# Kernel optimization log

Measured on AMD Instinct MI355X. Metric: run time of the kernel, lower is better.

The kernel has to match this reference:

```python
import jax, jax.numpy as jnp
import numpy as np

NUM_HEADS = 8
RMS_EPS = 1e-8


def rmsnorm(x, g):
    return x * jax.lax.rsqrt(jnp.mean(x * x, axis=-1, keepdims=True) + RMS_EPS) * g


def activation_quant(x):
    # per-token int8 absmax quant
    scale = 127.0 / jnp.clip(jnp.max(jnp.abs(x), axis=-1, keepdims=True), 1e-5)
    return jnp.clip(jnp.round(x * scale), -128, 127) / scale


def weight_quant(w):
    # ternary (1.58-bit) mean-absmax quant
    scale = 1.0 / jnp.clip(jnp.mean(jnp.abs(w)), 1e-5)
    return jnp.clip(jnp.round(w * scale), -1, 1) / scale


def bitlinear(x, w, g):
    # BitLinear: RMSNorm -> STE-quantized activation @ STE-quantized ternary weight
    xn = rmsnorm(x, g)
    xq = xn + jax.lax.stop_gradient(activation_quant(xn) - xn)
    wq = w + jax.lax.stop_gradient(weight_quant(w) - w)
    return xq @ wq.T


def _attention_pass(q_in, ctx, Wq, gq, Wkv, gkv, A, Bm, mag, Wp, gp):
    B, Nq, C = q_in.shape
    H = NUM_HEADS
    hd = C // H
    scale = hd ** -0.5
    q_proj = bitlinear(q_in, Wq, gq)                       # [B,Nq,C]
    delta = (q_in @ A.T) @ Bm.T                            # DoRA low-rank delta [B,Nq,C]
    q = q_proj.reshape(B, Nq, H, hd).transpose(0, 2, 1, 3)  # [B,H,Nq,hd]
    d = delta.reshape(B, Nq, H, hd).transpose(0, 2, 1, 3)
    q_final = q + mag * d                                  # mag: [1,H,1,1]
    kv = bitlinear(ctx, Wkv, gkv)                          # [B,Nc,2C]
    k, v = jnp.split(kv, 2, axis=-1)
    Nc = ctx.shape[1]
    k = k.reshape(B, Nc, H, hd).transpose(0, 2, 1, 3)
    v = v.reshape(B, Nc, H, hd).transpose(0, 2, 1, 3)
    scores = jnp.einsum('bhqd,bhkd->bhqk', q_final, k) * scale
    out = jnp.einsum('bhqk,bhkd->bhqd', jax.nn.softmax(scores, axis=-1), v)
    out = out.transpose(0, 2, 1, 3).reshape(B, Nq, C)
    return bitlinear(out, Wp, gp)


def setup_inputs() -> dict:
    key = jax.random.key(0)
    ks = jax.random.split(key, 20)
    B, Nx, Nc, D, R = 4, 4096, 1024, 512, 16
    H = NUM_HEADS

    def rn(k, shape, s=0.02):
        return jax.random.normal(k, shape, dtype=jnp.float32) * s

    return {
        'x': jax.random.normal(ks[0], (B, Nx, D), dtype=jnp.float32),
        'c': jax.random.normal(ks[1], (B, Nc, D), dtype=jnp.float32),
        # x-queries-on-c pass
        'W_qx': rn(ks[2], (D, D)), 'g_qx': jnp.ones((D,), jnp.float32),
        'W_kvc': rn(ks[3], (2 * D, D)), 'g_kvc': jnp.ones((D,), jnp.float32),
        'A_x': rn(ks[4], (R, D)), 'B_x': rn(ks[5], (D, R)),
        'mag_x': jnp.ones((1, H, 1, 1), jnp.float32),
        'W_px': rn(ks[6], (D, D)), 'g_px': jnp.ones((D,), jnp.float32),
        # c-queries-on-x pass
        'W_qc': rn(ks[7], (D, D)), 'g_qc': jnp.ones((D,), jnp.float32),
        'W_kvx': rn(ks[8], (2 * D, D)), 'g_kvx': jnp.ones((D,), jnp.float32),
        'A_c': rn(ks[9], (R, D)), 'B_c': rn(ks[10], (D, R)),
        'mag_c': jnp.ones((1, H, 1, 1), jnp.float32),
        'W_pc': rn(ks[11], (D, D)), 'g_pc': jnp.ones((D,), jnp.float32),
    }


def reference(x, c, W_qx, g_qx, W_kvc, g_kvc, A_x, B_x, mag_x, W_px, g_px,
              W_qc, g_qc, W_kvx, g_kvx, A_c, B_c, mag_c, W_pc, g_pc):
    x_out = x + _attention_pass(x, c, W_qx, g_qx, W_kvc, g_kvc, A_x, B_x, mag_x, W_px, g_px)
    c_out = c + _attention_pass(c, x, W_qc, g_qc, W_kvx, g_kvx, A_c, B_c, mag_c, W_pc, g_pc)
    return (x_out, c_out)
```

## Files before the change

### kernel.cpp

```cpp
#include <hip/hip_runtime.h>
#include <math.h>

#define DD 512
#define NHEAD 8
#define HDIM 64

typedef __bf16 bf16x8 __attribute__((ext_vector_type(8)));
typedef unsigned short u16x8 __attribute__((ext_vector_type(8)));
typedef float f32x4 __attribute__((ext_vector_type(4)));

#if __has_builtin(__builtin_amdgcn_exp2f)
#define EXP2F(x) __builtin_amdgcn_exp2f(x)
#else
#define EXP2F(x) exp2f(x)
#endif

#define QSCALE 0.18033688f

static __device__ __forceinline__ unsigned short f2bf(float f) {
    unsigned u = __builtin_bit_cast(unsigned, f);
    u += 0x7fffu + ((u >> 16) & 1u);
    return (unsigned short)(u >> 16);
}
static __device__ __forceinline__ float bf2f(unsigned short u) {
    return __builtin_bit_cast(float, (unsigned)u << 16);
}

static __device__ __forceinline__ float wsum32(const float* __restrict__ part, int mid) {
    int l = threadIdx.x & 63;
    float v = (l < 32) ? part[mid * 32 + l] : 0.f;
#pragma unroll
    for (int o = 16; o > 0; o >>= 1) v += __shfl_xor(v, o);
    return __shfl(v, 0);
}

#define GLOAD16(g, l)                                                          \
    __builtin_amdgcn_global_load_lds(                                          \
        (__attribute__((address_space(1))) void*)(g),                          \
        (__attribute__((address_space(3))) void*)(l), 16, 0, 0)

#define BSTEP(s, hc)                                                           \
    {                                                                          \
        _Pragma("unroll")                                                      \
        for (int i = 0; i < (hc); ++i) {                                       \
            float send = (lane & (s)) ? p[i] : p[i + (hc)];                    \
            float recv = __shfl_xor(send, (s));                                \
            p[i] = ((lane & (s)) ? p[i + (hc)] : p[i]) + recv;                 \
        }                                                                      \
    }

#define GEMM_KLOOP(Aq, Wq, m0, n0)                                             \
    {                                                                          \
        _Pragma("unroll")                                                      \
        for (int i = 0; i < 2; ++i) {                                          \
            int row = i * 64 + row_st;                                         \
            GLOAD16(Aq + (size_t)((m0) + row) * 512 + chunk * 8,               \
                    sA[0] + ((size_t)i * 256 + t) * 8);                        \
            GLOAD16(Wq + (size_t)((n0) + row) * 512 + chunk * 8,               \
                    sB[0] + ((size_t)i * 256 + t) * 8);                        \
        }                                                                      \
        asm volatile("s_waitcnt vmcnt(0)" ::: "memory");                       \
        __syncthreads();                                                       \
        int cur = 0;                                                           \
        for (int k0 = 0; k0 < 512; k0 += 32) {                                 \
            if (k0 + 32 < 512) {                                               \
                _Pragma("unroll")                                              \
                for (int i = 0; i < 2; ++i) {                                  \
                    int row = i * 64 + row_st;                                 \
                    GLOAD16(Aq + (size_t)((m0) + row) * 512 + k0 + 32 + chunk * 8, \
                            sA[cur ^ 1] + ((size_t)i * 256 + t) * 8);          \
                    GLOAD16(Wq + (size_t)((n0) + row) * 512 + k0 + 32 + chunk * 8, \
                            sB[cur ^ 1] + ((size_t)i * 256 + t) * 8);          \
                }                                                              \
            }                                                                  \
            bf16x8 af[4], bfr[4];                                              \
            _Pragma("unroll")                                                  \
            for (int mt = 0; mt < 4; ++mt)                                     \
                af[mt] = *reinterpret_cast<const bf16x8*>(                     \
                    &sA[cur][(wm * 64 + mt * 16 + lr) * 32 + lg * 8]);         \
            _Pragma("unroll")                                                  \
            for (int nt = 0; nt < 4; ++nt)                                     \
                bfr[nt] = *reinterpret_cast<const bf16x8*>(                    \
                    &sB[cur][(wn * 64 + nt * 16 + lr) * 32 + lg * 8]);         \
            __builtin_amdgcn_s_setprio(1);                                     \
            _Pragma("unroll")                                                  \
            for (int mt = 0; mt < 4; ++mt)                                     \
                _Pragma("unroll")                                              \
                for (int nt = 0; nt < 4; ++nt)                                 \
                    acc[mt][nt] = __builtin_amdgcn_mfma_f32_16x16x32_bf16(     \
                        af[mt], bfr[nt], acc[mt][nt], 0, 0, 0);                \
            __builtin_amdgcn_s_setprio(0);                                     \
            asm volatile("s_waitcnt vmcnt(0)" ::: "memory");                   \
            __syncthreads();                                                   \
            cur ^= 1;                                                          \
        }                                                                      \
    }

__global__ __launch_bounds__(256) void k_prep1(
    const float* __restrict__ W0, const float* __restrict__ W1,
    const float* __restrict__ W2, const float* __restrict__ W3,
    const float* __restrict__ W4, const float* __restrict__ W5,
    float* __restrict__ part,
    const float* __restrict__ x, const float* __restrict__ c,
    const float* __restrict__ g_qx, const float* __restrict__ g_kvx,
    const float* __restrict__ g_qc, const float* __restrict__ g_kvc,
    unsigned short* __restrict__ a_xq, unsigned short* __restrict__ a_xkv,
    unsigned short* __restrict__ a_cq, unsigned short* __restrict__ a_ckv,
    float* __restrict__ s_xq, float* __restrict__ s_xkv,
    float* __restrict__ s_cq, float* __restrict__ s_ckv,
    const float* __restrict__ A_x, const float* __restrict__ A_c,
    float* __restrict__ tmp_x, float* __restrict__ tmp_c) {
    int t = threadIdx.x;
    if (blockIdx.x < 192) {
        const float* Ws[6] = {W0, W1, W2, W3, W4, W5};
        const int cnt[6] = {262144, 524288, 262144, 262144, 524288, 262144};
        int mid = blockIdx.x >> 5, lb = blockIdx.x & 31;
        const float* W = Ws[mid];
        int n = cnt[mid];
        float s = 0.f;
        for (int i = lb * 256 + t; i < n; i += 32 * 256) s += fabsf(W[i]);
        __shared__ float red[4];
#pragma unroll
        for (int o = 32; o > 0; o >>= 1) s += __shfl_down(s, o);
        if ((t & 63) == 0) red[t >> 6] = s;
        __syncthreads();
        if (t == 0) part[blockIdx.x] = red[0] + red[1] + red[2] + red[3];
        return;
    }
    int w = t >> 6, lane = t & 63;
    int row = (int)(blockIdx.x - 192) * 4 + w;
    bool pc = (row >= 16384);
    int r = pc ? row - 16384 : row;
    const float* xr = (pc ? c : x) + (size_t)r * DD;
    const float* G1 = pc ? g_qc : g_qx;
    const float* G2 = pc ? g_kvc : g_kvx;
    unsigned short* O1 = pc ? a_cq : a_xq;
    unsigned short* O2 = pc ? a_ckv : a_xkv;
    float* S1 = pc ? s_cq : s_xq;
    float* S2 = pc ? s_ckv : s_xkv;
    const float* AM = pc ? A_c : A_x;
    float* TMP = pc ? tmp_c : tmp_x;

    float4 a = *(const float4*)(xr + lane * 8);
    float4 b = *(const float4*)(xr + lane * 8 + 4);
    float p[16];
#pragma unroll
    for (int cc = 0; cc < 16; ++cc) {
        const float4* ar = (const float4*)(AM + (size_t)cc * DD + lane * 8);
        float4 aa = ar[0], ab = ar[1];
        p[cc] = a.x*aa.x + a.y*aa.y + a.z*aa.z + a.w*aa.w
              + b.x*ab.x + b.y*ab.y + b.z*ab.z + b.w*ab.w;
    }
    BSTEP(1, 8) BSTEP(2, 4) BSTEP(4, 2) BSTEP(8, 1)
    p[0] += __shfl_xor(p[0], 16);
    p[0] += __shfl_xor(p[0], 32);
    if (lane < 16) {
        int cidx = ((lane & 1) << 3) | ((lane & 2) << 1) | ((lane & 4) >> 1) | ((lane & 8) >> 3);
        TMP[(size_t)r * 16 + cidx] = p[0];
    }
    float ss = a.x*a.x + a.y*a.y + a.z*a.z + a.w*a.w
             + b.x*b.x + b.y*b.y + b.z*b.z + b.w*b.w;
#pragma unroll
    for (int o = 32; o > 0; o >>= 1) ss += __shfl_xor(ss, o);
    float rn = 1.f / sqrtf(ss * (1.f / 512.f) + 1e-8f);
    const float* gs[2] = {G1, G2};
    unsigned short* os[2] = {O1, O2};
    float* scs[2] = {S1, S2};
#pragma unroll
    for (int pass = 0; pass < 2; ++pass) {
        float4 ga = *(const float4*)(gs[pass] + lane * 8);
        float4 gb = *(const float4*)(gs[pass] + lane * 8 + 4);
        float v[8] = {a.x*rn*ga.x, a.y*rn*ga.y, a.z*rn*ga.z, a.w*rn*ga.w,
                      b.x*rn*gb.x, b.y*rn*gb.y, b.z*rn*gb.z, b.w*rn*gb.w};
        float amax = 0.f;
#pragma unroll
        for (int i = 0; i < 8; ++i) amax = fmaxf(amax, fabsf(v[i]));
#pragma unroll
        for (int o = 32; o > 0; o >>= 1) amax = fmaxf(amax, __shfl_xor(amax, o));
        float mx = fmaxf(amax, 1e-5f);
        float scale = 127.f / mx;
        u16x8 qv;
#pragma unroll
        for (int i = 0; i < 8; ++i) {
            float tq = rintf(v[i] * scale);
            tq = fminf(fmaxf(tq, -128.f), 127.f);
            qv[i] = f2bf(tq);
        }
        *reinterpret_cast<u16x8*>(os[pass] + (size_t)r * DD + lane * 8) = qv;
        if (lane == 0) scs[pass][r] = mx / 127.f;
    }
}

__global__ __launch_bounds__(256) void k_prep2(
    const float* __restrict__ W0, const float* __restrict__ W1,
    const float* __restrict__ W2, const float* __restrict__ W3,
    const float* __restrict__ W4, const float* __restrict__ W5,
    const float* __restrict__ part, unsigned short* __restrict__ Wq,
    const float* __restrict__ tmp_x, const float* __restrict__ tmp_c,
    const float* __restrict__ B_x, const float* __restrict__ B_c,
    unsigned short* __restrict__ qf1, unsigned short* __restrict__ qf2) {
    if (blockIdx.x < 8192) {
        int e = blockIdx.x * 256 + threadIdx.x;
        const float* Ws[6] = {W0, W1, W2, W3, W4, W5};
        int mid, base;
        if (e < 262144)       { mid = 0; base = 0; }
        else if (e < 786432)  { mid = 1; base = 262144; }
        else if (e < 1048576) { mid = 2; base = 786432; }
        else if (e < 1310720) { mid = 3; base = 1048576; }
        else if (e < 1835008) { mid = 4; base = 1310720; }
        else                  { mid = 5; base = 1835008; }
        float cnt = (mid == 1 || mid == 4) ? 524288.f : 262144.f;
        float mean = fmaxf(wsum32(part, mid) / cnt, 1e-5f);
        float sc = 1.f / mean;
        float t = rintf(Ws[mid][e - base] * sc);
        t = fminf(fmaxf(t, -1.f), 1.f);
        Wq[e] = f2bf(t);
        return;
    }
    int idx = (int)(blockIdx.x - 8192) * 256 + threadIdx.x;
    int m2 = idx >> 9, n2 = idx & 511;
    const float* tr;
    const float* br;
    unsigned short* out;
    if (m2 < 16384) {
        tr = tmp_x + (size_t)m2 * 16; br = B_x + (size_t)n2 * 16; out = qf1 + idx;
    } else {
        tr = tmp_c + (size_t)(m2 - 16384) * 16; br = B_c + (size_t)n2 * 16;
        out = qf2 + (idx - 8388608);
    }
    const float4* t4 = (const float4*)tr;
    const float4* b4 = (const float4*)br;
    float acc = 0.f;
#pragma unroll
    for (int rr = 0; rr < 4; ++rr) {
        float4 ta = t4[rr], ba = b4[rr];
        acc += ta.x*ba.x + ta.y*ba.y + ta.z*ba.z + ta.w*ba.w;
    }
    *out = f2bf(acc);
}

__global__ __launch_bounds__(256) void k_rmsq_combine(
    const unsigned short* __restrict__ Op_a, const float* __restrict__ Lp_a,
    const float* __restrict__ g_a, unsigned short* __restrict__ out_a,
    float* __restrict__ sc_a,
    const unsigned short* __restrict__ Op_b, const float* __restrict__ Lp_b,
    const float* __restrict__ g_b, unsigned short* __restrict__ out_b,
    float* __restrict__ sc_b) {
    int w = threadIdx.x >> 6, lane = threadIdx.x & 63;
    int row = (int)blockIdx.x * 4 + w;
    bool pb = (row >= 16384);
    int r = pb ? row - 16384 : row;
    int S = pb ? 4 : 1;
    int lognq = pb ? 10 : 12;
    const unsigned short* Op = pb ? Op_b : Op_a;
    const float* Lp = pb ? Lp_b : Lp_a;
    const float* g  = pb ? g_b : g_a;
    unsigned short* out = pb ? out_b : out_a;
    float* a_inv = pb ? sc_b : sc_a;

    int Nq = 1 << lognq;
    int b = r >> lognq, q = r & (Nq - 1);
    int h = lane >> 3;
    float l = 0.f;
    float u[8] = {};
    for (int s = 0; s < S; ++s) {
        l += Lp[((size_t)(s * 4 + b) * 8 + h) * Nq + q];
        u16x8 ov = *reinterpret_cast<const u16x8*>(
            Op + ((size_t)(s * 4 + b) * Nq + q) * 512 + lane * 8);
#pragma unroll
        for (int i = 0; i < 8; ++i) u[i] += bf2f(ov[i]);
    }
    float invl = 1.f / l;
#pragma unroll
    for (int i = 0; i < 8; ++i) u[i] *= invl;
    float ss = 0.f;
#pragma unroll
    for (int i = 0; i < 8; ++i) ss += u[i] * u[i];
#pragma unroll
    for (int o = 32; o > 0; o >>= 1) ss += __shfl_xor(ss, o);
    float rn = 1.f / sqrtf(ss * (1.f / 512.f) + 1e-8f);
    float4 ga = *(const float4*)(g + lane * 8);
    float4 gb = *(const float4*)(g + lane * 8 + 4);
    float v[8] = {u[0]*rn*ga.x, u[1]*rn*ga.y, u[2]*rn*ga.z, u[3]*rn*ga.w,
                  u[4]*rn*gb.x, u[5]*rn*gb.y, u[6]*rn*gb.z, u[7]*rn*gb.w};
    float amax = 0.f;
#pragma unroll
    for (int i = 0; i < 8; ++i) amax = fmaxf(amax, fabsf(v[i]));
#pragma unroll
    for (int o = 32; o > 0; o >>= 1) amax = fmaxf(amax, __shfl_xor(amax, o));
    float mx = fmaxf(amax, 1e-5f);
    float scale = 127.f / mx;
    u16x8 qv;
#pragma unroll
    for (int i = 0; i < 8; ++i) {
        float tq = rintf(v[i] * scale);
        tq = fminf(fmaxf(tq, -128.f), 127.f);
        qv[i] = f2bf(tq);
    }
    *reinterpret_cast<u16x8*>(out + (size_t)r * DD + lane * 8) = qv;
    if (lane == 0) a_inv[r] = mx / 127.f;
}

__global__ __launch_bounds__(256) void k_gemm_qkv(
    const unsigned short* __restrict__ a3_a, const unsigned short* __restrict__ a3_b,
    const unsigned short* __restrict__ w3_a, const unsigned short* __restrict__ w3_b,
    const float* __restrict__ ai3_a, const float* __restrict__ ai3_b,
    const float* __restrict__ mag_a, const float* __restrict__ mag_b,
    const unsigned short* __restrict__ dl_a, const unsigned short* __restrict__ dl_b,
    unsigned short* __restrict__ Qb_a, unsigned short* __restrict__ Qb_b,
    const unsigned short* __restrict__ a4_a, const unsigned short* __restrict__ a4_b,
    const unsigned short* __restrict__ w4_a, const unsigned short* __restrict__ w4_b,
    const float* __restrict__ ai4_a, const float* __restrict__ ai4_b,
    unsigned short* __restrict__ Kb_a, unsigned short* __restrict__ Kb_b,
    unsigned short* __restrict__ Vt_a, unsigned short* __restrict__ Vt_b,
    const float* __restrict__ part) {
    __shared__ __align__(16) unsigned short sA[2][128 * 32];
    __shared__ __align__(16) unsigned short sB[2][128 * 32];
    int bid = blockIdx.x;
    bool isQ = (bid >= 1280);
    const unsigned short *Aq, *Wq;
    const float* a_inv;
    int m0, n0, logn, mid;
    float cnt;
    bool pb;
    if (!isQ) {
        int g = bid & 7, k = bid >> 3;
        n0 = (k & 7) * 128;
        int my = (k >> 3) * 8 + g;
        pb = my >= 32;
        m0 = (pb ? my - 32 : my) * 128;
        Aq = pb ? a4_b : a4_a;  Wq = pb ? w4_b : w4_a;
        a_inv = pb ? ai4_b : ai4_a;
        logn = pb ? 12 : 10;
        mid = pb ? 4 : 1; cnt = 524288.f;
    } else {
        int b2 = bid - 1280;
        int g = b2 & 7, k = b2 >> 3;
        n0 = (k & 3) * 128;
        int my = (k >> 2) * 8 + g;
        pb = my >= 128;
        m0 = (pb ? my - 128 : my) * 128;
        Aq = pb ? a3_b : a3_a;  Wq = pb ? w3_b : w3_a;
        a_inv = pb ? ai3_b : ai3_a;
        logn = pb ? 10 : 12;
        mid = pb ? 3 : 0; cnt = 262144.f;
    }
    float wv = fmaxf(wsum32(part, mid) / cnt, 1e-5f);

    int t = threadIdx.x;
    int w = t >> 6, lane = t & 63;
    int wm = w >> 1, wn = w & 1;
    int lr = lane & 15, lg = lane >> 4;
    int row_st = t >> 2, chunk = t & 3;
    f32x4 acc[4][4] = {};

    GEMM_KLOOP(Aq, Wq, m0, n0)

    if (!isQ) {
        unsigned short* OutB = pb ? Kb_b : Kb_a;
        unsigned short* OutB2 = pb ? Vt_b : Vt_a;
        const bool isV = (n0 >= 512);
        const int Nc = 1 << logn;
#pragma unroll
        for (int mt = 0; mt < 4; ++mt) {
            int mb = m0 + wm * 64 + mt * 16 + lg * 4;
            int b = mb >> logn, key = mb & (Nc - 1);
            float as_[4];
#pragma unroll
            for (int r = 0; r < 4; ++r) as_[r] = a_inv[mb + r] * wv;
#pragma unroll
            for (int nt = 0; nt < 4; ++nt) {
                int n = n0 + wn * 64 + nt * 16 + lr;
                int n2 = isV ? (n - 512) : n;
                int h = n2 >> 6, dd = n2 & 63;
                if (isV) {
                    int i0 = key & 31;
                    int keyp = (key & ~31) | (((i0 >> 2) & 3) * 8 + ((i0 >> 4) & 1) * 4);
                    ushort4 v;
                    v.x = f2bf(acc[mt][nt][0] * as_[0]);
                    v.y = f2bf(acc[mt][nt][1] * as_[1]);
                    v.z = f2bf(acc[mt][nt][2] * as_[2]);
                    v.w = f2bf(acc[mt][nt][3] * as_[3]);
                    *reinterpret_cast<ushort4*>(
                        OutB2 + ((size_t)(b * NHEAD + h) * 64 + dd) * Nc + keyp) = v;
                } else {
#pragma unroll
                    for (int r = 0; r < 4; ++r)
                        OutB[((size_t)(b * NHEAD + h) * Nc + key + r) * 64 + dd] =
                            f2bf(acc[mt][nt][r] * as_[r]);
                }
            }
        }
    } else {
        const float* Extra = pb ? mag_b : mag_a;
        const unsigned short* Dlt = pb ? dl_b : dl_a;
        unsigned short* OutB = pb ? Qb_b : Qb_a;
#pragma unroll
        for (int mt = 0; mt < 4; ++mt) {
#pragma unroll
            for (int r = 0; r < 4; ++r) {
                int m = m0 + wm * 64 + mt * 16 + lg * 4 + r;
                float as = a_inv[m] * wv;
                int b = m >> logn, q = m & ((1 << logn) - 1);
#pragma unroll
                for (int nt = 0; nt < 4; ++nt) {
                    int n = n0 + wn * 64 + nt * 16 + lr;
                    float dl = bf2f(Dlt[(size_t)m * 512 + n]);
                    float val = acc[mt][nt][r] * as + Extra[n >> 6] * dl;
                    int h = n >> 6, d = n & 63;
                    OutB[((((size_t)(b * NHEAD + h)) << logn) + q) * 64 + d] =
                        f2bf(val * QSCALE);
                }
            }
        }
    }
}

__global__ __launch_bounds__(256) void k_gemm_out(
    const unsigned short* __restrict__ a_a, const unsigned short* __restrict__ a_b,
    const unsigned short* __restrict__ w_a, const unsigned short* __restrict__ w_b,
    const float* __restrict__ ai_a, const float* __restrict__ ai_b,
    const float* __restrict__ part,
    const float* __restrict__ Ex_a, const float* __restrict__ Ex_b,
    float* __restrict__ OF_a, float* __restrict__ OF_b) {
    __shared__ __align__(16) unsigned short sA[2][128 * 32];
    __shared__ __align__(16) unsigned short sB[2][128 * 32];
    int bid = blockIdx.x;
    int g = bid & 7, k = bid >> 3;
    int n0 = (k & 3) * 128;
    int my = (k >> 2) * 8 + g;
    bool pb = (my >= 128);
    int m0 = (pb ? my - 128 : my) * 128;
    const unsigned short* Aq = pb ? a_b : a_a;
    const unsigned short* Wq = pb ? w_b : w_a;
    const float* a_inv = pb ? ai_b : ai_a;
    const float* Extra = pb ? Ex_b : Ex_a;
    float* OutF = pb ? OF_b : OF_a;
    float wv = fmaxf(wsum32(part, pb ? 5 : 2) / 262144.f, 1e-5f);

    int t = threadIdx.x;
    int w = t >> 6, lane = t & 63;
    int wm = w >> 1, wn = w & 1;
    int lr = lane & 15, lg = lane >> 4;
    int row_st = t >> 2, chunk = t & 3;
    f32x4 acc[4][4] = {};

    GEMM_KLOOP(Aq, Wq, m0, n0)

#pragma unroll
    for (int mt = 0; mt < 4; ++mt) {
#pragma unroll
        for (int r = 0; r < 4; ++r) {
            int m = m0 + wm * 64 + mt * 16 + lg * 4 + r;
            float as = a_inv[m] * wv;
#pragma unroll
            for (int nt = 0; nt < 4; ++nt) {
                int n = n0 + wn * 64 + nt * 16 + lr;
                size_t idx = (size_t)m * 512 + n;
                OutF[idx] = acc[mt][nt][r] * as + Extra[idx];
            }
        }
    }
}

__global__ __launch_bounds__(512) void k_attn_mfma(
    const unsigned short* __restrict__ Qb_a, const unsigned short* __restrict__ Kb_a,
    const unsigned short* __restrict__ Vt_a, unsigned short* __restrict__ Op_a,
    float* __restrict__ Lp_a,
    const unsigned short* __restrict__ Qb_b, const unsigned short* __restrict__ Kb_b,
    const unsigned short* __restrict__ Vt_b, unsigned short* __restrict__ Op_b,
    float* __restrict__ Lp_b) {
    __shared__ unsigned short sK[2][64][72];
    __shared__ unsigned short sVt[2][64][72];
    int t = threadIdx.x;
    int w = t >> 6, lane = t & 63;
    int lr = lane & 15, lg = lane >> 4;

    int bid = blockIdx.x;
    bool pb = (bid < 512);
    int lb = pb ? bid : bid - 512;
    const unsigned short* Qb = pb ? Qb_b : Qb_a;
    const unsigned short* Kb = pb ? Kb_b : Kb_a;
    const unsigned short* Vt = pb ? Vt_b : Vt_a;
    unsigned short* Opart = pb ? Op_b : Op_a;
    float* Lpart = pb ? Lp_b : Lp_a;
    int Nq = pb ? 1024 : 4096;
    int Nc = pb ? 4096 : 1024;
    int S = pb ? 4 : 1;
    int LOGS = pb ? 2 : 0;
    int nqs = pb ? 2 : 4;

    int j = lb >> 3;
    int s = j & (S - 1);
    int j2 = j >> LOGS;
    int qblk = j2 & ((1 << nqs) - 1);
    int bh = ((lb & 7) << 2) | (j2 >> nqs);
    int b = bh >> 3, h = bh & 7;
    int q0 = qblk * 256 + w * 32;

    bf16x8 aq[2][2];
#pragma unroll
    for (int qt = 0; qt < 2; ++qt) {
        const unsigned short* qbase = Qb + ((size_t)bh * Nq + q0 + qt * 16 + lr) * 64 + lg * 8;
        aq[qt][0] = *reinterpret_cast<const bf16x8*>(qbase);
        aq[qt][1] = *reinterpret_cast<const bf16x8*>(qbase + 32);
    }

    u16x8 ou;
#pragma unroll
    for (int jj = 0; jj < 8; ++jj) ou[jj] = (lr == 0) ? 0x3F80 : 0;
    bf16x8 onesf = __builtin_bit_cast(bf16x8, ou);

    f32x4 o[2][4] = {};
    f32x4 osum[2] = {};

    const unsigned short* kglob = Kb + (size_t)bh * Nc * 64;
    const unsigned short* vglob = Vt + (size_t)bh * 64 * (size_t)Nc;

    int srow = t >> 3, sseg = t & 7;
    const unsigned short* kptr = kglob + (size_t)srow * 64 + sseg * 8;
    const unsigned short* vptr = vglob + (size_t)srow * Nc + sseg * 8;

    int kts = s * (Nc >> LOGS);
    int nt = (Nc >> LOGS) >> 6;

    bf16x8 rK = *reinterpret_cast<const bf16x8*>(kptr + (size_t)kts * 64);
    bf16x8 rV = *reinterpret_cast<const bf16x8*>(vptr + kts);
    *reinterpret_cast<bf16x8*>(&sK[0][srow][sseg * 8]) = rK;
    *reinterpret_cast<bf16x8*>(&sVt[0][srow][sseg * 8]) = rV;
    rK = *reinterpret_cast<const bf16x8*>(kptr + (size_t)(kts + 64) * 64);
    rV = *reinterpret_cast<const bf16x8*>(vptr + kts + 64);
    __syncthreads();

    int cur = 0;
    for (int ti = 0; ti < nt; ++ti) {
        if (ti + 1 < nt) {
            *reinterpret_cast<bf16x8*>(&sK[cur ^ 1][srow][sseg * 8]) = rK;
            *reinterpret_cast<bf16x8*>(&sVt[cur ^ 1][srow][sseg * 8]) = rV;
            if (ti + 2 < nt) {
                int knext = kts + (ti + 2) * 64;
                rK = *reinterpret_cast<const bf16x8*>(kptr + (size_t)knext * 64);
                rV = *reinterpret_cast<const bf16x8*>(vptr + knext);
            }
        }
#pragma unroll
        for (int half = 0; half < 2; ++half) {
            bf16x8 pa0, pa1;
#pragma unroll
            for (int ki = 0; ki < 2; ++ki) {
                int kt = half * 2 + ki;
                bf16x8 bk0 = *reinterpret_cast<const bf16x8*>(&sK[cur][kt * 16 + lr][lg * 8]);
                bf16x8 bk1 = *reinterpret_cast<const bf16x8*>(&sK[cur][kt * 16 + lr][32 + lg * 8]);
                f32x4 a0 = {}, a1 = {};
                __builtin_amdgcn_s_setprio(1);
                a0 = __builtin_amdgcn_mfma_f32_16x16x32_bf16(bk0, aq[0][0], a0, 0, 0, 0);
                a1 = __builtin_amdgcn_mfma_f32_16x16x32_bf16(bk0, aq[1][0], a1, 0, 0, 0);
                a0 = __builtin_amdgcn_mfma_f32_16x16x32_bf16(bk1, aq[0][1], a0, 0, 0, 0);
                a1 = __builtin_amdgcn_mfma_f32_16x16x32_bf16(bk1, aq[1][1], a1, 0, 0, 0);
                __builtin_amdgcn_s_setprio(0);
                const int hb = ki * 4;
#pragma unroll
                for (int r = 0; r < 4; ++r) {
                    pa0[hb + r] = (__bf16)EXP2F(a0[r]);
                    pa1[hb + r] = (__bf16)EXP2F(a1[r]);
                }
            }
            __builtin_amdgcn_s_setprio(1);
#pragma unroll
            for (int dt = 0; dt < 4; ++dt) {
                bf16x8 vb = *reinterpret_cast<const bf16x8*>(&sVt[cur][dt * 16 + lr][half * 32 + lg * 8]);
                o[0][dt] = __builtin_amdgcn_mfma_f32_16x16x32_bf16(pa0, vb, o[0][dt], 0, 0, 0);
                o[1][dt] = __builtin_amdgcn_mfma_f32_16x16x32_bf16(pa1, vb, o[1][dt], 0, 0, 0);
            }
            osum[0] = __builtin_amdgcn_mfma_f32_16x16x32_bf16(pa0, onesf, osum[0], 0, 0, 0);
            osum[1] = __builtin_amdgcn_mfma_f32_16x16x32_bf16(pa1, onesf, osum[1], 0, 0, 0);
            __builtin_amdgcn_s_setprio(0);
        }
        __syncthreads();
        cur ^= 1;
    }
    unsigned short* obase = Opart + ((size_t)(s * 4 + b) * Nq + q0) * 512 + h * 64;
#pragma unroll
    for (int qt = 0; qt < 2; ++qt)
#pragma unroll
        for (int dt = 0; dt < 4; ++dt)
#pragma unroll
            for (int r = 0; r < 4; ++r)
                obase[(size_t)(qt * 16 + lg * 4 + r) * 512 + dt * 16 + lr] = f2bf(o[qt][dt][r]);
    if (lr == 0) {
        float* lbase = Lpart + ((size_t)(s * 4 + b) * 8 + h) * Nq + q0;
#pragma unroll
        for (int qt = 0; qt < 2; ++qt)
#pragma unroll
            for (int r = 0; r < 4; ++r)
                lbase[qt * 16 + lg * 4 + r] = osum[qt][r];
    }
}

extern "C" void kernel_launch(void* const* d_in, const int* in_sizes, int n_in,
                              void* d_out, int out_size, void* d_ws, size_t ws_size,
                              hipStream_t stream) {
    const float* x     = (const float*)d_in[0];
    const float* c     = (const float*)d_in[1];
    const float* Wq_x  = (const float*)d_in[2];
    const float* g_qx  = (const float*)d_in[3];
    const float* Wkv_c = (const float*)d_in[4];
    const float* g_kvc = (const float*)d_in[5];
    const float* A_x   = (const float*)d_in[6];
    const float* B_x   = (const float*)d_in[7];
    const float* mag_x = (const float*)d_in[8];
    const float* Wp_x  = (const float*)d_in[9];
    const float* g_px  = (const float*)d_in[10];
    const float* Wq_c  = (const float*)d_in[11];
    const float* g_qc  = (const float*)d_in[12];
    const float* Wkv_x = (const float*)d_in[13];
    const float* g_kvx = (const float*)d_in[14];
    const float* A_c   = (const float*)d_in[15];
    const float* B_c   = (const float*)d_in[16];
    const float* mag_c = (const float*)d_in[17];
    const float* Wp_c  = (const float*)d_in[18];
    const float* g_pc  = (const float*)d_in[19];

    float* ws = (float*)d_ws;
    unsigned short* Wb = (unsigned short*)ws;
    const size_t Woff[6] = {0, 262144, 786432, 1048576, 1310720, 1835008};
    float* part  = ws + 1048576;
    float* sc_xq  = ws + 1049600;
    float* sc_xkv = sc_xq + 16384;
    float* sc_cq  = sc_xkv + 16384;
    float* sc_ckv = sc_cq + 4096;
    float* sc_o1  = sc_ckv + 4096;
    float* sc_o2  = sc_o1 + 16384;
    float* tmp_x  = ws + 1111040;
    float* tmp_c  = tmp_x + 262144;
    float* actblk = ws + 1438720;
    unsigned short* act_xq  = (unsigned short*)actblk;
    unsigned short* act_xkv = (unsigned short*)(actblk + 4194304);
    unsigned short* act_cq  = (unsigned short*)(actblk + 8388608);
    unsigned short* act_ckv = (unsigned short*)(actblk + 9437184);
    unsigned short* Opart1 = (unsigned short*)actblk;
    float* qf1_f  = ws + 11924480;
    unsigned short* Opart2 = (unsigned short*)qf1_f;
    float* qf2_f  = ws + 16118784;
    float* Qb1_f  = ws + 17167360;
    float* Qb2_f  = ws + 21361664;
    float* Kb1_f  = ws + 22410240;
    float* Vt1_f  = ws + 23458816;
    float* Kb2_f  = ws + 24507392;
    float* Vt2_f  = ws + 28701696;
    float* Lpart1 = ws + 32896000;
    float* Lpart2 = ws + 33027072;

    unsigned short* qf1 = (unsigned short*)qf1_f;
    unsigned short* qf2 = (unsigned short*)qf2_f;
    unsigned short* Qb1 = (unsigned short*)Qb1_f;
    unsigned short* Qb2 = (unsigned short*)Qb2_f;
    unsigned short* Kb1 = (unsigned short*)Kb1_f;
    unsigned short* Vt1 = (unsigned short*)Vt1_f;
    unsigned short* Kb2 = (unsigned short*)Kb2_f;
    unsigned short* Vt2 = (unsigned short*)Vt2_f;
    unsigned short* act_o1 = Qb1;
    unsigned short* act_o2 = Qb2;

    size_t need = (size_t)33158144 * sizeof(float);
    if (ws_size < need) return;

    float* outx = (float*)d_out;
    float* outc = outx + (size_t)4 * 4096 * 512;

    k_prep1<<<5312, 256, 0, stream>>>(Wq_x, Wkv_c, Wp_x, Wq_c, Wkv_x, Wp_c, part,
                                      x, c, g_qx, g_kvx, g_qc, g_kvc,
                                      act_xq, act_xkv, act_cq, act_ckv,
                                      sc_xq, sc_xkv, sc_cq, sc_ckv,
                                      A_x, A_c, tmp_x, tmp_c);
    k_prep2<<<49152, 256, 0, stream>>>(Wq_x, Wkv_c, Wp_x, Wq_c, Wkv_x, Wp_c, part, Wb,
                                       tmp_x, tmp_c, B_x, B_c, qf1, qf2);
    k_gemm_qkv<<<1920, 256, 0, stream>>>(
        act_xq, act_cq, Wb + Woff[0], Wb + Woff[3], sc_xq, sc_cq,
        mag_x, mag_c, qf1, qf2, Qb1, Qb2,
        act_ckv, act_xkv, Wb + Woff[1], Wb + Woff[4], sc_ckv, sc_xkv,
        Kb1, Kb2, Vt1, Vt2, part);
    k_attn_mfma<<<1024, 512, 0, stream>>>(Qb1, Kb1, Vt1, Opart1, Lpart1,
                                          Qb2, Kb2, Vt2, Opart2, Lpart2);
    k_rmsq_combine<<<5120, 256, 0, stream>>>(Opart1, Lpart1, g_px, act_o1, sc_o1,
                                             Opart2, Lpart2, g_pc, act_o2, sc_o2);
    k_gemm_out<<<640, 256, 0, stream>>>(
        act_o1, act_o2, Wb + Woff[2], Wb + Woff[5], sc_o1, sc_o2, part,
        x, c, outx, outc);
}
```

Baseline: 271.4 us.

## Switch BitLinear GEMMs from bf16 to int8 MFMA with int8 activations and weights

Stores quantized activations and ternary weights as int8 instead of bf16, and replaces the bf16 16x16x32 MFMA k-loop with the i32 16x16x64 int8 MFMA, using K steps of 64. This halves the global and LDS bytes per GEMM tile, halves the number of k-iterations, and uses the higher int8 matrix throughput. Integer accumulators are converted to float in the epilogues. The results stay exact because the quantized values are small integers, but the GEMMs may be only part of total time next to attention.

```diff
diff --git a/kernel.cpp b/kernel.cpp
--- a/kernel.cpp
+++ b/kernel.cpp
@@ -8,6 +8,8 @@
 typedef __bf16 bf16x8 __attribute__((ext_vector_type(8)));
 typedef unsigned short u16x8 __attribute__((ext_vector_type(8)));
 typedef float f32x4 __attribute__((ext_vector_type(4)));
+typedef int i32x4 __attribute__((ext_vector_type(4)));
+typedef signed char i8x8 __attribute__((ext_vector_type(8)));
 
 #if __has_builtin(__builtin_amdgcn_exp2f)
 #define EXP2F(x) __builtin_amdgcn_exp2f(x)
@@ -49,45 +51,43 @@
         }                                                                      \
     }
 
-#define GEMM_KLOOP(Aq, Wq, m0, n0)                                             \
+#define GEMM_KLOOP_I8(Aq, Wq, m0, n0)                                          \
     {                                                                          \
         _Pragma("unroll")                                                      \
         for (int i = 0; i < 2; ++i) {                                          \
-            int row = i * 64 + row_st;                                         \
-            GLOAD16(Aq + (size_t)((m0) + row) * 512 + chunk * 8,               \
-                    sA[0] + ((size_t)i * 256 + t) * 8);                        \
-            GLOAD16(Wq + (size_t)((n0) + row) * 512 + chunk * 8,               \
-                    sB[0] + ((size_t)i * 256 + t) * 8);                        \
+            GLOAD16(Aq + (size_t)((m0) + i * 64 + row_st) * 512 + chunk * 16,  \
+                    sA[0] + ((size_t)i * 256 + t) * 16);                       \
+            GLOAD16(Wq + (size_t)((n0) + i * 64 + row_st) * 512 + chunk * 16,  \
+                    sB[0] + ((size_t)i * 256 + t) * 16);                       \
         }                                                                      \
         asm volatile("s_waitcnt vmcnt(0)" ::: "memory");                       \
         __syncthreads();                                                       \
         int cur = 0;                                                           \
-        for (int k0 = 0; k0 < 512; k0 += 32) {                                 \
-            if (k0 + 32 < 512) {                                               \
+        for (int k0 = 0; k0 < 512; k0 += 64) {                                 \
+            if (k0 + 64 < 512) {                                               \
                 _Pragma("unroll")                                              \
                 for (int i = 0; i < 2; ++i) {                                  \
-                    int row = i * 64 + row_st;                                 \
-                    GLOAD16(Aq + (size_t)((m0) + row) * 512 + k0 + 32 + chunk * 8, \
-                            sA[cur ^ 1] + ((size_t)i * 256 + t) * 8);          \
-                    GLOAD16(Wq + (size_t)((n0) + row) * 512 + k0 + 32 + chunk * 8, \
-                            sB[cur ^ 1] + ((size_t)i * 256 + t) * 8);          \
+                    GLOAD16(Aq + (size_t)((m0) + i * 64 + row_st) * 512 + k0 + 64 + chunk * 16, \
+                            sA[cur ^ 1] + ((size_t)i * 256 + t) * 16);         \
+                    GLOAD16(Wq + (size_t)((n0) + i * 64 + row_st) * 512 + k0 + 64 + chunk * 16, \
+                            sB[cur ^ 1] + ((size_t)i * 256 + t) * 16);         \
                 }                                                              \
             }                                                                  \
-            bf16x8 af[4], bfr[4];                                              \
+            i32x4 af[4], bfr[4];                                               \
             _Pragma("unroll")                                                  \
             for (int mt = 0; mt < 4; ++mt)                                     \
-                af[mt] = *reinterpret_cast<const bf16x8*>(                     \
-                    &sA[cur][(wm * 64 + mt * 16 + lr) * 32 + lg * 8]);         \
+                af[mt] = *reinterpret_cast<const i32x4*>(                      \
+                    &sA[cur][(wm * 64 + mt * 16 + lr) * 64 + lg * 16]);        \
             _Pragma("unroll")                                                  \
             for (int nt = 0; nt < 4; ++nt)                                     \
-                bfr[nt] = *reinterpret_cast<const bf16x8*>(                    \
-                    &sB[cur][(wn * 64 + nt * 16 + lr) * 32 + lg * 8]);         \
+                bfr[nt] = *reinterpret_cast<const i32x4*>(                     \
+                    &sB[cur][(wn * 64 + nt * 16 + lr) * 64 + lg * 16]);        \
             __builtin_amdgcn_s_setprio(1);                                     \
             _Pragma("unroll")                                                  \
             for (int mt = 0; mt < 4; ++mt)                                     \
                 _Pragma("unroll")                                              \
                 for (int nt = 0; nt < 4; ++nt)                                 \
-                    acc[mt][nt] = __builtin_amdgcn_mfma_f32_16x16x32_bf16(     \
+                    acc[mt][nt] = __builtin_amdgcn_mfma_i32_16x16x64_i8(       \
                         af[mt], bfr[nt], acc[mt][nt], 0, 0, 0);                \
             __builtin_amdgcn_s_setprio(0);                                     \
             asm volatile("s_waitcnt vmcnt(0)" ::: "memory");                   \
@@ -104,8 +104,8 @@
     const float* __restrict__ x, const float* __restrict__ c,
     const float* __restrict__ g_qx, const float* __restrict__ g_kvx,
     const float* __restrict__ g_qc, const float* __restrict__ g_kvc,
-    unsigned short* __restrict__ a_xq, unsigned short* __restrict__ a_xkv,
-    unsigned short* __restrict__ a_cq, unsigned short* __restrict__ a_ckv,
+    signed char* __restrict__ a_xq, signed char* __restrict__ a_xkv,
+    signed char* __restrict__ a_cq, signed char* __restrict__ a_ckv,
     float* __restrict__ s_xq, float* __restrict__ s_xkv,
     float* __restrict__ s_cq, float* __restrict__ s_ckv,
     const float* __restrict__ A_x, const float* __restrict__ A_c,
@@ -134,8 +134,8 @@
     const float* xr = (pc ? c : x) + (size_t)r * DD;
     const float* G1 = pc ? g_qc : g_qx;
     const float* G2 = pc ? g_kvc : g_kvx;
-    unsigned short* O1 = pc ? a_cq : a_xq;
-    unsigned short* O2 = pc ? a_ckv : a_xkv;
+    signed char* O1 = pc ? a_cq : a_xq;
+    signed char* O2 = pc ? a_ckv : a_xkv;
     float* S1 = pc ? s_cq : s_xq;
     float* S2 = pc ? s_ckv : s_xkv;
     const float* AM = pc ? A_c : A_x;
@@ -164,7 +164,7 @@
     for (int o = 32; o > 0; o >>= 1) ss += __shfl_xor(ss, o);
     float rn = 1.f / sqrtf(ss * (1.f / 512.f) + 1e-8f);
     const float* gs[2] = {G1, G2};
-    unsigned short* os[2] = {O1, O2};
+    signed char* os[2] = {O1, O2};
     float* scs[2] = {S1, S2};
 #pragma unroll
     for (int pass = 0; pass < 2; ++pass) {
@@ -179,14 +179,14 @@
         for (int o = 32; o > 0; o >>= 1) amax = fmaxf(amax, __shfl_xor(amax, o));
         float mx = fmaxf(amax, 1e-5f);
         float scale = 127.f / mx;
-        u16x8 qv;
+        i8x8 qv;
 #pragma unroll
         for (int i = 0; i < 8; ++i) {
             float tq = rintf(v[i] * scale);
             tq = fminf(fmaxf(tq, -128.f), 127.f);
-            qv[i] = f2bf(tq);
+            qv[i] = (signed char)(int)tq;
         }
-        *reinterpret_cast<u16x8*>(os[pass] + (size_t)r * DD + lane * 8) = qv;
+        *reinterpret_cast<i8x8*>(os[pass] + (size_t)r * DD + lane * 8) = qv;
         if (lane == 0) scs[pass][r] = mx / 127.f;
     }
 }
@@ -195,7 +195,7 @@
     const float* __restrict__ W0, const float* __restrict__ W1,
     const float* __restrict__ W2, const float* __restrict__ W3,
     const float* __restrict__ W4, const float* __restrict__ W5,
-    const float* __restrict__ part, unsigned short* __restrict__ Wq,
+    const float* __restrict__ part, signed char* __restrict__ Wq,
     const float* __restrict__ tmp_x, const float* __restrict__ tmp_c,
     const float* __restrict__ B_x, const float* __restrict__ B_c,
     unsigned short* __restrict__ qf1, unsigned short* __restrict__ qf2) {
@@ -214,7 +214,7 @@
         float sc = 1.f / mean;
         float t = rintf(Ws[mid][e - base] * sc);
         t = fminf(fmaxf(t, -1.f), 1.f);
-        Wq[e] = f2bf(t);
+        Wq[e] = (signed char)(int)t;
         return;
     }
     int idx = (int)(blockIdx.x - 8192) * 256 + threadIdx.x;
@@ -241,10 +241,10 @@
 
 __global__ __launch_bounds__(256) void k_rmsq_combine(
     const unsigned short* __restrict__ Op_a, const float* __restrict__ Lp_a,
-    const float* __restrict__ g_a, unsigned short* __restrict__ out_a,
+    const float* __restrict__ g_a, signed char* __restrict__ out_a,
     float* __restrict__ sc_a,
     const unsigned short* __restrict__ Op_b, const float* __restrict__ Lp_b,
-    const float* __restrict__ g_b, unsigned short* __restrict__ out_b,
+    const float* __restrict__ g_b, signed char* __restrict__ out_b,
     float* __restrict__ sc_b) {
     int w = threadIdx.x >> 6, lane = threadIdx.x & 63;
     int row = (int)blockIdx.x * 4 + w;
@@ -255,7 +255,7 @@
     const unsigned short* Op = pb ? Op_b : Op_a;
     const float* Lp = pb ? Lp_b : Lp_a;
     const float* g  = pb ? g_b : g_a;
-    unsigned short* out = pb ? out_b : out_a;
+    signed char* out = pb ? out_b : out_a;
     float* a_inv = pb ? sc_b : sc_a;
 
     int Nq = 1 << lognq;
@@ -290,35 +290,35 @@
     for (int o = 32; o > 0; o >>= 1) amax = fmaxf(amax, __shfl_xor(amax, o));
     float mx = fmaxf(amax, 1e-5f);
     float scale = 127.f / mx;
-    u16x8 qv;
+    i8x8 qv;
 #pragma unroll
     for (int i = 0; i < 8; ++i) {
         float tq = rintf(v[i] * scale);
         tq = fminf(fmaxf(tq, -128.f), 127.f);
-        qv[i] = f2bf(tq);
-    }
-    *reinterpret_cast<u16x8*>(out + (size_t)r * DD + lane * 8) = qv;
+        qv[i] = (signed char)(int)tq;
+    }
+    *reinterpret_cast<i8x8*>(out + (size_t)r * DD + lane * 8) = qv;
     if (lane == 0) a_inv[r] = mx / 127.f;
 }
 
 __global__ __launch_bounds__(256) void k_gemm_qkv(
-    const unsigned short* __restrict__ a3_a, const unsigned short* __restrict__ a3_b,
-    const unsigned short* __restrict__ w3_a, const unsigned short* __restrict__ w3_b,
+    const signed char* __restrict__ a3_a, const signed char* __restrict__ a3_b,
+    const signed char* __restrict__ w3_a, const signed char* __restrict__ w3_b,
     const float* __restrict__ ai3_a, const float* __restrict__ ai3_b,
     const float* __restrict__ mag_a, const float* __restrict__ mag_b,
     const unsigned short* __restrict__ dl_a, const unsigned short* __restrict__ dl_b,
     unsigned short* __restrict__ Qb_a, unsigned short* __restrict__ Qb_b,
-    const unsigned short* __restrict__ a4_a, const unsigned short* __restrict__ a4_b,
-    const unsigned short* __restrict__ w4_a, const unsigned short* __restrict__ w4_b,
+    const signed char* __restrict__ a4_a, const signed char* __restrict__ a4_b,
+    const signed char* __restrict__ w4_a, const signed char* __restrict__ w4_b,
     const float* __restrict__ ai4_a, const float* __restrict__ ai4_b,
     unsigned short* __restrict__ Kb_a, unsigned short* __restrict__ Kb_b,
     unsigned short* __restrict__ Vt_a, unsigned short* __restrict__ Vt_b,
     const float* __restrict__ part) {
-    __shared__ __align__(16) unsigned short sA[2][128 * 32];
-    __shared__ __align__(16) unsigned short sB[2][128 * 32];
+    __shared__ __align__(16) unsigned char sA[2][128 * 64];
+    __shared__ __align__(16) unsigned char sB[2][128 * 64];
     int bid = blockIdx.x;
     bool isQ = (bid >= 1280);
-    const unsigned short *Aq, *Wq;
+    const signed char *Aq, *Wq;
     const float* a_inv;
     int m0, n0, logn, mid;
     float cnt;
@@ -352,9 +352,9 @@
     int wm = w >> 1, wn = w & 1;
     int lr = lane & 15, lg = lane >> 4;
     int row_st = t >> 2, chunk = t & 3;
-    f32x4 acc[4][4] = {};
-
-    GEMM_KLOOP(Aq, Wq, m0, n0)
+    i32x4 acc[4][4] = {};
+
+    GEMM_KLOOP_I8(Aq, Wq, m0, n0)
 
     if (!isQ) {
         unsigned short* OutB = pb ? Kb_b : Kb_a;
@@ -377,17 +377,17 @@
                     int i0 = key & 31;
                     int keyp = (key & ~31) | (((i0 >> 2) & 3) * 8 + ((i0 >> 4) & 1) * 4);
                     ushort4 v;
-                    v.x = f2bf(acc[mt][nt][0] * as_[0]);
-                    v.y = f2bf(acc[mt][nt][1] * as_[1]);
-                    v.z = f2bf(acc[mt][nt][2] * as_[2]);
-                    v.w = f2bf(acc[mt][nt][3] * as_[3]);
+                    v.x = f2bf((float)acc[mt][nt][0] * as_[0]);
+                    v.y = f2bf((float)acc[mt][nt][1] * as_[1]);
+                    v.z = f2bf((float)acc[mt][nt][2] * as_[2]);
+                    v.w = f2bf((float)acc[mt][nt][3] * as_[3]);
                     *reinterpret_cast<ushort4*>(
                         OutB2 + ((size_t)(b * NHEAD + h) * 64 + dd) * Nc + keyp) = v;
                 } else {
 #pragma unroll
                     for (int r = 0; r < 4; ++r)
                         OutB[((size_t)(b * NHEAD + h) * Nc + key + r) * 64 + dd] =
-                            f2bf(acc[mt][nt][r] * as_[r]);
+                            f2bf((float)acc[mt][nt][r] * as_[r]);
                 }
             }
         }
@@ -406,7 +406,7 @@
                 for (int nt = 0; nt < 4; ++nt) {
                     int n = n0 + wn * 64 + nt * 16 + lr;
                     float dl = bf2f(Dlt[(size_t)m * 512 + n]);
-                    float val = acc[mt][nt][r] * as + Extra[n >> 6] * dl;
+                    float val = (float)acc[mt][nt][r] * as + Extra[n >> 6] * dl;
                     int h = n >> 6, d = n & 63;
                     OutB[((((size_t)(b * NHEAD + h)) << logn) + q) * 64 + d] =
                         f2bf(val * QSCALE);
@@ -417,22 +417,22 @@
 }
 
 __global__ __launch_bounds__(256) void k_gemm_out(
-    const unsigned short* __restrict__ a_a, const unsigned short* __restrict__ a_b,
-    const unsigned short* __restrict__ w_a, const unsigned short* __restrict__ w_b,
+    const signed char* __restrict__ a_a, const signed char* __restrict__ a_b,
+    const signed char* __restrict__ w_a, const signed char* __restrict__ w_b,
     const float* __restrict__ ai_a, const float* __restrict__ ai_b,
     const float* __restrict__ part,
     const float* __restrict__ Ex_a, const float* __restrict__ Ex_b,
     float* __restrict__ OF_a, float* __restrict__ OF_b) {
-    __shared__ __align__(16) unsigned short sA[2][128 * 32];
-    __shared__ __align__(16) unsigned short sB[2][128 * 32];
+    __shared__ __align__(16) unsigned char sA[2][128 * 64];
+    __shared__ __align__(16) unsigned char sB[2][128 * 64];
     int bid = blockIdx.x;
     int g = bid & 7, k = bid >> 3;
     int n0 = (k & 3) * 128;
     int my = (k >> 2) * 8 + g;
     bool pb = (my >= 128);
     int m0 = (pb ? my - 128 : my) * 128;
-    const unsigned short* Aq = pb ? a_b : a_a;
-    const unsigned short* Wq = pb ? w_b : w_a;
+    const signed char* Aq = pb ? a_b : a_a;
+    const signed char* Wq = pb ? w_b : w_a;
     const float* a_inv = pb ? ai_b : ai_a;
     const float* Extra = pb ? Ex_b : Ex_a;
     float* OutF = pb ? OF_b : OF_a;
@@ -443,9 +443,9 @@
     int wm = w >> 1, wn = w & 1;
     int lr = lane & 15, lg = lane >> 4;
     int row_st = t >> 2, chunk = t & 3;
-    f32x4 acc[4][4] = {};
-
-    GEMM_KLOOP(Aq, Wq, m0, n0)
+    i32x4 acc[4][4] = {};
+
+    GEMM_KLOOP_I8(Aq, Wq, m0, n0)
 
 #pragma unroll
     for (int mt = 0; mt < 4; ++mt) {
@@ -457,7 +457,7 @@
             for (int nt = 0; nt < 4; ++nt) {
                 int n = n0 + wn * 64 + nt * 16 + lr;
                 size_t idx = (size_t)m * 512 + n;
-                OutF[idx] = acc[mt][nt][r] * as + Extra[idx];
+                OutF[idx] = (float)acc[mt][nt][r] * as + Extra[idx];
             }
         }
     }
@@ -622,7 +622,7 @@
     const float* g_pc  = (const float*)d_in[19];
 
     float* ws = (float*)d_ws;
-    unsigned short* Wb = (unsigned short*)ws;
+    signed char* Wb = (signed char*)ws;
     const size_t Woff[6] = {0, 262144, 786432, 1048576, 1310720, 1835008};
     float* part  = ws + 1048576;
     float* sc_xq  = ws + 1049600;
@@ -634,10 +634,10 @@
     float* tmp_x  = ws + 1111040;
     float* tmp_c  = tmp_x + 262144;
     float* actblk = ws + 1438720;
-    unsigned short* act_xq  = (unsigned short*)actblk;
-    unsigned short* act_xkv = (unsigned short*)(actblk + 4194304);
-    unsigned short* act_cq  = (unsigned short*)(actblk + 8388608);
-    unsigned short* act_ckv = (unsigned short*)(actblk + 9437184);
+    signed char* act_xq  = (signed char*)actblk;
+    signed char* act_xkv = (signed char*)(actblk + 4194304);
+    signed char* act_cq  = (signed char*)(actblk + 8388608);
+    signed char* act_ckv = (signed char*)(actblk + 9437184);
     unsigned short* Opart1 = (unsigned short*)actblk;
     float* qf1_f  = ws + 11924480;
     unsigned short* Opart2 = (unsigned short*)qf1_f;
@@ -659,8 +659,8 @@
     unsigned short* Vt1 = (unsigned short*)Vt1_f;
     unsigned short* Kb2 = (unsigned short*)Kb2_f;
     unsigned short* Vt2 = (unsigned short*)Vt2_f;
-    unsigned short* act_o1 = Qb1;
-    unsigned short* act_o2 = Qb2;
+    signed char* act_o1 = (signed char*)Qb1;
+    signed char* act_o2 = (signed char*)Qb2;
 
     size_t need = (size_t)33158144 * sizeof(float);
     if (ws_size < need) return;
```

Result: faster. 245.0 us (-9.7%).
